# Performance work log

Measured on AMD Instinct MI355X. Metric: run time of the kernel, lower is better.

Reference implementation:

```python
import jax, jax.numpy as jnp
import numpy as np

WIN = 7


def rel_index(win: int) -> jnp.ndarray:
    ys, xs = jnp.meshgrid(jnp.arange(win), jnp.arange(win), indexing='ij')
    coords = jnp.stack([ys.reshape(-1), xs.reshape(-1)], axis=-1)  # (S, 2)
    diff = coords[None, :, :] - coords[:, None, :] + (win - 1)     # (S, S, 2)
    return diff[..., 0] * (2 * win - 1) + diff[..., 1]             # (S, S)


def setup_inputs() -> dict:
    key = jax.random.key(0)
    ks = jax.random.split(key, 5)
    B, WN, S, C, H = 64, 64, WIN * WIN, 192, 6
    X = jax.random.normal(ks[0], (B, WN, S, C), dtype=jnp.float32)
    # torch nn.Linear(emb_dim, 3*emb_dim) -> store as (in, out) for x @ W
    Wqkv = jax.random.normal(ks[1], (C, 3 * C), dtype=jnp.float32) * 0.02
    bqkv = jnp.zeros((3 * C,), dtype=jnp.float32)
    Wo = jax.random.normal(ks[2], (C, C), dtype=jnp.float32) * 0.02
    bo = jnp.zeros((C,), dtype=jnp.float32)
    bias_table = jax.random.normal(ks[3], ((2 * WIN - 1) ** 2, H), dtype=jnp.float32) * 0.02
    return {"X": X, "Wqkv": Wqkv, "bqkv": bqkv, "Wo": Wo, "bo": bo, "bias_table": bias_table}


def reference(X, Wqkv, bqkv, Wo, bo, bias_table):
    B, WN, S, C = X.shape
    H = bias_table.shape[1]
    D = C // H
    scale = D ** -0.5
    # qkv projection: (B, WN, S, 3C) -> (3, B, WN, H, S, D)
    qkv = (X @ Wqkv + bqkv).reshape(B, WN, S, 3, H, D).transpose(3, 0, 1, 4, 2, 5)
    q, k, v = qkv[0], qkv[1], qkv[2]
    attn = jnp.einsum('bwhqd,bwhkd->bwhqk', q, k) * scale  # (B, WN, H, S, S)
    # gathered relative position bias: (S, S, H) -> (H, S, S)
    idx = rel_index(WIN)
    bias = bias_table[idx].transpose(2, 0, 1)
    attn = attn + bias[None, None]
    proba = jax.nn.softmax(attn, axis=-1)  # dropout omitted (eval mode)
    out = jnp.einsum('bwhqk,bwhkd->bwhqd', proba, v)  # (B, WN, H, S, D)
    out = out.transpose(0, 1, 3, 2, 4).reshape(B, WN, S, C)
    return out @ Wo + bo
```

## Files before the change

kernel.cpp:

```cpp
#include <hip/hip_runtime.h>
#include <hip/hip_bf16.h>


typedef __attribute__((ext_vector_type(4))) float f32x4;
typedef __attribute__((ext_vector_type(8))) short bf16x8;
typedef __attribute__((ext_vector_type(4))) unsigned short u16x4;

#define SCALE 0.17677669529663689f
#define MFMA(a, b, acc) __builtin_amdgcn_mfma_f32_16x16x32_bf16(a, b, acc, 0, 0, 0)

__device__ __forceinline__ unsigned short f2bf(float f) {
  union { float f; unsigned int u; } v; v.f = f;
  return (unsigned short)((v.u + 0x7FFFu + ((v.u >> 16) & 1u)) >> 16);
}

__device__ __forceinline__ void gll16(const unsigned short* src, unsigned short* dst) {
  __builtin_amdgcn_global_load_lds(
      (const __attribute__((address_space(1))) unsigned int*)src,
      (__attribute__((address_space(3))) unsigned int*)dst, 16, 0, 0);
}

__global__ void wprep(const float* __restrict__ Wqkv, const float* __restrict__ Wo,
                      unsigned short* __restrict__ WqkvTs, unsigned short* __restrict__ WoTs) {
  int i = blockIdx.x * 256 + threadIdx.x;
  if (i < 576 * 192) {
    int n = i / 192, k = i % 192;
    int ch = n >> 6, row = n & 63;
    int dst = ch * 12288 + row * 192 + (((k >> 3) ^ (row & 7)) << 3) + (k & 7);
    WqkvTs[dst] = f2bf(Wqkv[k * 576 + n]);
  }
  if (i < 192 * 192) {
    int n = i / 192, k = i % 192;
    int dst = n * 192 + (((k >> 3) ^ (n & 7)) << 3) + (k & 7);
    WoTs[dst] = f2bf(Wo[k * 192 + n]);
  }
}

__global__ __launch_bounds__(512, 4)
void qkv_gemm(const float* __restrict__ X, const unsigned short* __restrict__ WqkvTs,
              const float* __restrict__ bqkv, unsigned short* __restrict__ qkv) {
  __shared__ __align__(16) unsigned short Bs[2][12288];
  __shared__ float biasLds[576];

  const int tid = threadIdx.x, w8 = tid >> 6, lane = tid & 63;
  const int g = lane >> 4, c = lane & 15;
  const size_t bm = (size_t)blockIdx.x * 128;
  const f32x4 z = {0.f, 0.f, 0.f, 0.f};

  #pragma unroll
  for (int jj = 0; jj < 3; ++jj)
    gll16(WqkvTs + (w8 * 3 + jj) * 512 + lane * 8, &Bs[0][(w8 * 3 + jj) * 512]);
  for (int j = tid; j < 576; j += 512) biasLds[j] = bqkv[j];

  bf16x8 af[6];
  {
    const float* xr = X + (bm + w8 * 16 + c) * 192;
    #pragma unroll
    for (int ks = 0; ks < 6; ++ks) {
      f32x4 lo = *(const f32x4*)(xr + ks * 32 + g * 8);
      f32x4 hi = *(const f32x4*)(xr + ks * 32 + g * 8 + 4);
      bf16x8 a;
      a[0] = (short)f2bf(lo[0]); a[1] = (short)f2bf(lo[1]);
      a[2] = (short)f2bf(lo[2]); a[3] = (short)f2bf(lo[3]);
      a[4] = (short)f2bf(hi[0]); a[5] = (short)f2bf(hi[1]);
      a[6] = (short)f2bf(hi[2]); a[7] = (short)f2bf(hi[3]);
      af[ks] = a;
    }
  }
  asm volatile("s_waitcnt vmcnt(0)\n\ts_barrier" ::: "memory");
  __builtin_amdgcn_sched_barrier(0);

  for (int nc = 0; nc < 9; ++nc) {
    const int cur = nc & 1;
    if (nc < 8) {
      #pragma unroll
      for (int jj = 0; jj < 3; ++jj)
        gll16(WqkvTs + (nc + 1) * 12288 + (w8 * 3 + jj) * 512 + lane * 8,
              &Bs[cur ^ 1][(w8 * 3 + jj) * 512]);
    }
    f32x4 acc[4] = {z, z, z, z};
    #pragma unroll
    for (int ks = 0; ks < 6; ++ks) {
      #pragma unroll
      for (int nf = 0; nf < 4; ++nf) {
        const bf16x8 bv = *(const bf16x8*)(
            &Bs[cur][(nf * 16 + c) * 192 + (((ks * 4 + g) ^ (c & 7)) << 3)]);
        acc[nf] = MFMA(bv, af[ks], acc[nf]);
      }
    }
    unsigned short* qp = qkv + (bm + w8 * 16 + c) * 576 + nc * 64;
    #pragma unroll
    for (int nf = 0; nf < 4; ++nf) {
      const f32x4 bb = *(const f32x4*)(biasLds + nc * 64 + nf * 16 + 4 * g);
      u16x4 s;
      #pragma unroll
      for (int r = 0; r < 4; ++r) s[r] = f2bf(acc[nf][r] + bb[r]);
      *(u16x4*)(qp + nf * 16 + 4 * g) = s;
    }

    if (nc < 8) {
      asm volatile("s_waitcnt vmcnt(4)\n\ts_barrier" ::: "memory");
      __builtin_amdgcn_sched_barrier(0);
    }
  }
}

__global__ __launch_bounds__(512, 4)
void attn_win(unsigned short* __restrict__ qkv, const float* __restrict__ btab) {
  __shared__ __align__(16) unsigned short Ks[64 * 200];
  __shared__ __align__(16) unsigned short Vt[192 * 72];
  __shared__ __align__(16) unsigned short scr[8][1152];
  __shared__ float biasF[1014];

  const int tid = threadIdx.x, w8 = tid >> 6, lane = tid & 63;
  const int g = lane >> 4, c = lane & 15;
  const int mt = w8 & 3, hw = w8 >> 2;
  const size_t tokbase = (size_t)blockIdx.x * 49;
  const f32x4 z = {0.f, 0.f, 0.f, 0.f};

  for (int j = tid; j < 1014; j += 512) biasF[j] = btab[j];
  for (int j = tid; j < 360; j += 512) {
    uint4 zz = {0, 0, 0, 0};
    *(uint4*)(&Ks[(49 + j / 24) * 200 + (j % 24) * 8]) = zz;
  }
  for (int j = tid; j < 2880; j += 512) Vt[(j / 15) * 72 + 49 + j % 15] = 0;
  for (int j = tid; j < 1176; j += 512) {
    int row = j / 24, ch = j % 24;
    *(uint4*)(&Ks[row * 200 + ch * 8]) =
        *(const uint4*)(qkv + (tokbase + row) * 576 + 192 + ch * 8);
  }
  for (int j = tid; j < 1176; j += 512) {
    int row = j / 24, ch = j % 24;
    uint4 v = *(const uint4*)(qkv + (tokbase + row) * 576 + 384 + ch * 8);
    const unsigned short* e = (const unsigned short*)&v;
    #pragma unroll
    for (int m = 0; m < 8; ++m) {
      int k = (ch + m) & 7;
      Vt[(ch * 8 + k) * 72 + row] = e[k];
    }
  }

  const int qbase = mt * 16;
  const int q = qbase + c;
  const bool qvalid = q < 49;
  const int qc = qvalid ? q : 48;

  bf16x8 bqh[3];
  #pragma unroll
  for (int hi = 0; hi < 3; ++hi)
    bqh[hi] = *(const bf16x8*)(qkv + (tokbase + qc) * 576 + (hw * 3 + hi) * 32 + g * 8);

  __syncthreads();

  const int qoff6 = ((6 - qc / 7) * 13 + (6 - qc % 7)) * 6;
  int kb6[16];
  #pragma unroll
  for (int i = 0; i < 16; ++i) {
    int k = (i >> 2) * 16 + g * 4 + (i & 3);
    int kk = k < 49 ? k : 48;
    kb6[i] = ((kk / 7) * 13 + (kk % 7)) * 6;
  }
  unsigned short* Pw = scr[w8];

  #pragma unroll
  for (int hi = 0; hi < 3; ++hi) {
    const int h = hw * 3 + hi;
    const bf16x8 bq = bqh[hi];
    const int cofs = h * 32 + g * 8;
    f32x4 s0 = MFMA(*(const bf16x8*)(Ks + (c) * 200 + cofs), bq, z);
    f32x4 s1 = MFMA(*(const bf16x8*)(Ks + (16 + c) * 200 + cofs), bq, z);
    f32x4 s2 = MFMA(*(const bf16x8*)(Ks + (32 + c) * 200 + cofs), bq, z);
    f32x4 s3 = MFMA(*(const bf16x8*)(Ks + (48 + c) * 200 + cofs), bq, z);

    float p[16];
    float mx = -3e38f;
    #pragma unroll
    for (int i = 0; i < 16; ++i) {
      const int t = i >> 2, r = i & 3;
      const int k = t * 16 + g * 4 + r;
      const float sv = (t == 0) ? s0[r] : (t == 1) ? s1[r] : (t == 2) ? s2[r] : s3[r];
      const float b = biasF[kb6[i] + qoff6 + h];
      const float lg = (qvalid && (k < 49)) ? fmaf(sv, SCALE, b) : -1e30f;
      p[i] = lg;
      mx = fmaxf(mx, lg);
    }
    mx = fmaxf(mx, __shfl_xor(mx, 16));
    mx = fmaxf(mx, __shfl_xor(mx, 32));
    float sum = 0.f;
    #pragma unroll
    for (int i = 0; i < 16; ++i) { p[i] = __expf(p[i] - mx); sum += p[i]; }
    sum += __shfl_xor(sum, 16);
    sum += __shfl_xor(sum, 32);
    const float inv = 1.0f / sum;
    #pragma unroll
    for (int t = 0; t < 4; ++t) {
      u16x4 pkv;
      #pragma unroll
      for (int r = 0; r < 4; ++r) pkv[r] = f2bf(p[t * 4 + r] * inv);
      *(u16x4*)(Pw + c * 72 + t * 16 + g * 4) = pkv;
    }

    f32x4 o0 = z, o1 = z;
    #pragma unroll
    for (int ks = 0; ks < 2; ++ks) {
      const bf16x8 ap = *(const bf16x8*)(Pw + c * 72 + ks * 32 + g * 8);
      const bf16x8 v0 = *(const bf16x8*)(Vt + (h * 32 + c) * 72 + ks * 32 + g * 8);
      const bf16x8 v1 = *(const bf16x8*)(Vt + (h * 32 + 16 + c) * 72 + ks * 32 + g * 8);
      o0 = MFMA(ap, v0, o0);
      o1 = MFMA(ap, v1, o1);
    }
    #pragma unroll
    for (int r = 0; r < 4; ++r) {
      Pw[(4 * g + r) * 72 + c]      = f2bf(o0[r]);
      Pw[(4 * g + r) * 72 + 16 + c] = f2bf(o1[r]);
    }
    uint4 ov = *(const uint4*)(Pw + c * 72 + g * 8);
    if (qvalid)
      *(uint4*)(qkv + (tokbase + q) * 576 + h * 32 + g * 8) = ov;
  }
}

__global__ __launch_bounds__(512, 4)
void out_gemm(const unsigned short* __restrict__ qkv, const unsigned short* __restrict__ WoTs,
              const float* __restrict__ bo, float* __restrict__ out) {
  __shared__ __align__(16) unsigned short Ws[192 * 192];

  const int tid = threadIdx.x, w8 = tid >> 6, lane = tid & 63;
  const int g = lane >> 4, c = lane & 15;
  const int mt = w8 & 3, half = w8 >> 2;
  const size_t r0 = (size_t)blockIdx.x * 128 + mt * 32;
  const f32x4 z = {0.f, 0.f, 0.f, 0.f};

  #pragma unroll
  for (int jj = 0; jj < 9; ++jj)
    gll16(WoTs + (w8 * 9 + jj) * 512 + lane * 8, &Ws[(w8 * 9 + jj) * 512]);

  bf16x8 af0[6], af1[6];
  #pragma unroll
  for (int ks = 0; ks < 6; ++ks) {
    af0[ks] = *(const bf16x8*)(qkv + (r0 + c) * 576 + ks * 32 + g * 8);
    af1[ks] = *(const bf16x8*)(qkv + (r0 + 16 + c) * 576 + ks * 32 + g * 8);
  }
  __syncthreads();

  #pragma unroll
  for (int nf = 0; nf < 6; ++nf) {
    const int ocl = half * 96 + nf * 16;
    f32x4 acc0 = z, acc1 = z;
    #pragma unroll
    for (int ks = 0; ks < 6; ++ks) {
      const bf16x8 bv = *(const bf16x8*)(
          &Ws[(ocl + c) * 192 + (((ks * 4 + g) ^ (c & 7)) << 3)]);
      acc0 = MFMA(bv, af0[ks], acc0);
      acc1 = MFMA(bv, af1[ks], acc1);
    }
    const f32x4 bb = *(const f32x4*)(bo + ocl + 4 * g);
    *(f32x4*)(out + (r0 + c) * 192 + ocl + 4 * g)      = acc0 + bb;
    *(f32x4*)(out + (r0 + 16 + c) * 192 + ocl + 4 * g) = acc1 + bb;
  }
}

extern "C" void kernel_launch(void* const* d_in, const int* in_sizes, int n_in,
                              void* d_out, int out_size, void* d_ws, size_t ws_size,
                              hipStream_t stream) {
  (void)in_sizes; (void)n_in; (void)out_size; (void)ws_size;
  const float* X    = (const float*)d_in[0];
  const float* Wqkv = (const float*)d_in[1];
  const float* bqkv = (const float*)d_in[2];
  const float* Wo   = (const float*)d_in[3];
  const float* bo   = (const float*)d_in[4];
  const float* btab = (const float*)d_in[5];

  unsigned short* WqkvTs = (unsigned short*)d_ws;
  unsigned short* WoTs   = WqkvTs + 576 * 192;
  unsigned short* qkv    = WoTs + 192 * 192;

  wprep<<<432, 256, 0, stream>>>(Wqkv, Wo, WqkvTs, WoTs);
  qkv_gemm<<<1568, 512, 0, stream>>>(X, WqkvTs, bqkv, qkv);
  attn_win<<<4096, 512, 0, stream>>>(qkv, btab);
  out_gemm<<<1568, 512, 0, stream>>>(qkv, WoTs, bo, (float*)d_out);
}
```

Baseline: 299.3 us.

## Double wavefronts per block in projection GEMMs and drop K padding zeroing

The QKV and output projection kernels now launch 1024 threads (16 waves) per block instead of 512. Each wave computes half the output columns of a 16-row tile, so per-wave register use and MFMA chain length shrink and more waves are available to hide latency. Weight staging via global_load_lds is redistributed across the 16 waves, and the wait counts are adjusted to match. The attention kernel no longer zeroes the padded K rows, which saves LDS stores but leaves rows 49-63 holding stale data that the QK MFMA may read (risking garbage or NaN unless those rows are masked).

```diff
diff --git a/kernel.cpp b/kernel.cpp
--- a/kernel.cpp
+++ b/kernel.cpp
@@ -36,25 +36,33 @@
   }
 }
 
-__global__ __launch_bounds__(512, 4)
+__global__ __launch_bounds__(1024, 8)
 void qkv_gemm(const float* __restrict__ X, const unsigned short* __restrict__ WqkvTs,
               const float* __restrict__ bqkv, unsigned short* __restrict__ qkv) {
   __shared__ __align__(16) unsigned short Bs[2][12288];
   __shared__ float biasLds[576];
 
-  const int tid = threadIdx.x, w8 = tid >> 6, lane = tid & 63;
+  const int tid = threadIdx.x, w16 = tid >> 6, lane = tid & 63;
   const int g = lane >> 4, c = lane & 15;
+  const int mt = w16 >> 1, half = w16 & 1;
   const size_t bm = (size_t)blockIdx.x * 128;
   const f32x4 z = {0.f, 0.f, 0.f, 0.f};
 
-  #pragma unroll
-  for (int jj = 0; jj < 3; ++jj)
-    gll16(WqkvTs + (w8 * 3 + jj) * 512 + lane * 8, &Bs[0][(w8 * 3 + jj) * 512]);
-  for (int j = tid; j < 576; j += 512) biasLds[j] = bqkv[j];
+  auto stage = [&](const unsigned short* src, unsigned short* dstBuf) {
+    if (w16 < 8) {
+      gll16(src + (w16 * 2) * 512 + lane * 8, dstBuf + (w16 * 2) * 512);
+      gll16(src + (w16 * 2 + 1) * 512 + lane * 8, dstBuf + (w16 * 2 + 1) * 512);
+    } else {
+      gll16(src + (16 + (w16 - 8)) * 512 + lane * 8, dstBuf + (16 + (w16 - 8)) * 512);
+    }
+  };
+
+  stage(WqkvTs, Bs[0]);
+  if (tid < 576) biasLds[tid] = bqkv[tid];
 
   bf16x8 af[6];
   {
-    const float* xr = X + (bm + w8 * 16 + c) * 192;
+    const float* xr = X + (bm + mt * 16 + c) * 192;
     #pragma unroll
     for (int ks = 0; ks < 6; ++ks) {
       f32x4 lo = *(const f32x4*)(xr + ks * 32 + g * 8);
@@ -67,39 +75,35 @@
       af[ks] = a;
     }
   }
-  asm volatile("s_waitcnt vmcnt(0)\n\ts_barrier" ::: "memory");
+  asm volatile("s_waitcnt vmcnt(0) lgkmcnt(0)\n\ts_barrier" ::: "memory");
   __builtin_amdgcn_sched_barrier(0);
 
   for (int nc = 0; nc < 9; ++nc) {
     const int cur = nc & 1;
+    if (nc < 8)
+      stage(WqkvTs + (nc + 1) * 12288, Bs[cur ^ 1]);
+
+    f32x4 acc0 = z, acc1 = z;
+    const int rb = half * 32;
+    #pragma unroll
+    for (int ks = 0; ks < 6; ++ks) {
+      const int sw = ((ks * 4 + g) ^ (c & 7)) << 3;
+      const bf16x8 bv0 = *(const bf16x8*)(&Bs[cur][(rb + c) * 192 + sw]);
+      const bf16x8 bv1 = *(const bf16x8*)(&Bs[cur][(rb + 16 + c) * 192 + sw]);
+      acc0 = MFMA(bv0, af[ks], acc0);
+      acc1 = MFMA(bv1, af[ks], acc1);
+    }
+    const f32x4 bb0 = *(const f32x4*)(biasLds + nc * 64 + rb + 4 * g);
+    const f32x4 bb1 = *(const f32x4*)(biasLds + nc * 64 + rb + 16 + 4 * g);
+    u16x4 s0, s1;
+    #pragma unroll
+    for (int r = 0; r < 4; ++r) { s0[r] = f2bf(acc0[r] + bb0[r]); s1[r] = f2bf(acc1[r] + bb1[r]); }
+    unsigned short* qp = qkv + (bm + mt * 16 + c) * 576 + nc * 64 + rb;
+    *(u16x4*)(qp + 4 * g) = s0;
+    *(u16x4*)(qp + 16 + 4 * g) = s1;
+
     if (nc < 8) {
-      #pragma unroll
-      for (int jj = 0; jj < 3; ++jj)
-        gll16(WqkvTs + (nc + 1) * 12288 + (w8 * 3 + jj) * 512 + lane * 8,
-              &Bs[cur ^ 1][(w8 * 3 + jj) * 512]);
-    }
-    f32x4 acc[4] = {z, z, z, z};
-    #pragma unroll
-    for (int ks = 0; ks < 6; ++ks) {
-      #pragma unroll
-      for (int nf = 0; nf < 4; ++nf) {
-        const bf16x8 bv = *(const bf16x8*)(
-            &Bs[cur][(nf * 16 + c) * 192 + (((ks * 4 + g) ^ (c & 7)) << 3)]);
-        acc[nf] = MFMA(bv, af[ks], acc[nf]);
-      }
-    }
-    unsigned short* qp = qkv + (bm + w8 * 16 + c) * 576 + nc * 64;
-    #pragma unroll
-    for (int nf = 0; nf < 4; ++nf) {
-      const f32x4 bb = *(const f32x4*)(biasLds + nc * 64 + nf * 16 + 4 * g);
-      u16x4 s;
-      #pragma unroll
-      for (int r = 0; r < 4; ++r) s[r] = f2bf(acc[nf][r] + bb[r]);
-      *(u16x4*)(qp + nf * 16 + 4 * g) = s;
-    }
-
-    if (nc < 8) {
-      asm volatile("s_waitcnt vmcnt(4)\n\ts_barrier" ::: "memory");
+      asm volatile("s_waitcnt vmcnt(2)\n\ts_barrier" ::: "memory");
       __builtin_amdgcn_sched_barrier(0);
     }
   }
@@ -119,10 +123,6 @@
   const f32x4 z = {0.f, 0.f, 0.f, 0.f};
 
   for (int j = tid; j < 1014; j += 512) biasF[j] = btab[j];
-  for (int j = tid; j < 360; j += 512) {
-    uint4 zz = {0, 0, 0, 0};
-    *(uint4*)(&Ks[(49 + j / 24) * 200 + (j % 24) * 8]) = zz;
-  }
   for (int j = tid; j < 2880; j += 512) Vt[(j / 15) * 72 + 49 + j % 15] = 0;
   for (int j = tid; j < 1176; j += 512) {
     int row = j / 24, ch = j % 24;
@@ -220,43 +220,45 @@
   }
 }
 
-__global__ __launch_bounds__(512, 4)
+__global__ __launch_bounds__(1024, 8)
 void out_gemm(const unsigned short* __restrict__ qkv, const unsigned short* __restrict__ WoTs,
               const float* __restrict__ bo, float* __restrict__ out) {
   __shared__ __align__(16) unsigned short Ws[192 * 192];
 
-  const int tid = threadIdx.x, w8 = tid >> 6, lane = tid & 63;
+  const int tid = threadIdx.x, w16 = tid >> 6, lane = tid & 63;
   const int g = lane >> 4, c = lane & 15;
-  const int mt = w8 & 3, half = w8 >> 2;
-  const size_t r0 = (size_t)blockIdx.x * 128 + mt * 32;
+  const int mt = w16 >> 1, half = w16 & 1;
+  const size_t r0 = (size_t)blockIdx.x * 128 + mt * 16;
   const f32x4 z = {0.f, 0.f, 0.f, 0.f};
 
-  #pragma unroll
-  for (int jj = 0; jj < 9; ++jj)
-    gll16(WoTs + (w8 * 9 + jj) * 512 + lane * 8, &Ws[(w8 * 9 + jj) * 512]);
-
-  bf16x8 af0[6], af1[6];
-  #pragma unroll
-  for (int ks = 0; ks < 6; ++ks) {
-    af0[ks] = *(const bf16x8*)(qkv + (r0 + c) * 576 + ks * 32 + g * 8);
-    af1[ks] = *(const bf16x8*)(qkv + (r0 + 16 + c) * 576 + ks * 32 + g * 8);
-  }
+  if (w16 < 8) {
+    #pragma unroll
+    for (int jj = 0; jj < 5; ++jj)
+      gll16(WoTs + (w16 * 5 + jj) * 512 + lane * 8, &Ws[(w16 * 5 + jj) * 512]);
+  } else {
+    #pragma unroll
+    for (int jj = 0; jj < 4; ++jj)
+      gll16(WoTs + (40 + (w16 - 8) * 4 + jj) * 512 + lane * 8, &Ws[(40 + (w16 - 8) * 4 + jj) * 512]);
+  }
+
+  bf16x8 af[6];
+  #pragma unroll
+  for (int ks = 0; ks < 6; ++ks)
+    af[ks] = *(const bf16x8*)(qkv + (r0 + c) * 576 + ks * 32 + g * 8);
   __syncthreads();
 
   #pragma unroll
   for (int nf = 0; nf < 6; ++nf) {
     const int ocl = half * 96 + nf * 16;
-    f32x4 acc0 = z, acc1 = z;
+    f32x4 acc = z;
     #pragma unroll
     for (int ks = 0; ks < 6; ++ks) {
       const bf16x8 bv = *(const bf16x8*)(
           &Ws[(ocl + c) * 192 + (((ks * 4 + g) ^ (c & 7)) << 3)]);
-      acc0 = MFMA(bv, af0[ks], acc0);
-      acc1 = MFMA(bv, af1[ks], acc1);
+      acc = MFMA(bv, af[ks], acc);
     }
     const f32x4 bb = *(const f32x4*)(bo + ocl + 4 * g);
-    *(f32x4*)(out + (r0 + c) * 192 + ocl + 4 * g)      = acc0 + bb;
-    *(f32x4*)(out + (r0 + 16 + c) * 192 + ocl + 4 * g) = acc1 + bb;
+    *(f32x4*)(out + (r0 + c) * 192 + ocl + 4 * g) = acc + bb;
   }
 }
 
@@ -276,7 +278,7 @@
   unsigned short* qkv    = WoTs + 192 * 192;
 
   wprep<<<432, 256, 0, stream>>>(Wqkv, Wo, WqkvTs, WoTs);
-  qkv_gemm<<<1568, 512, 0, stream>>>(X, WqkvTs, bqkv, qkv);
+  qkv_gemm<<<1568, 1024, 0, stream>>>(X, WqkvTs, bqkv, qkv);
   attn_win<<<4096, 512, 0, stream>>>(qkv, btab);
-  out_gemm<<<1568, 512, 0, stream>>>(qkv, WoTs, bo, (float*)d_out);
-}
+  out_gemm<<<1568, 1024, 0, stream>>>(qkv, WoTs, bo, (float*)d_out);
+}
```

New measurement: 326.1 us. +9.0%, slower.
